# Performance work log

Measured on AMD Instinct MI355X. Metric: run time of the kernel, lower is better.

The kernel has to match this reference:

```python
import jax, jax.numpy as jnp
import numpy as np

HEADS = 4  # opt['heads']; attention_dim=128 -> d_k=32


def setup_inputs() -> dict:
    key = jax.random.key(0)
    ks = jax.random.split(key, 8)
    N, E, IN_F, ATT = 50000, 1600000, 256, 128
    x = jax.random.normal(ks[0], (N, IN_F), dtype=jnp.float32)
    edge = jax.random.randint(ks[1], (2, E), 0, N, dtype=jnp.int64)
    Qw = jax.random.normal(ks[2], (ATT, IN_F), dtype=jnp.float32) * 0.02
    Qb = jax.random.normal(ks[3], (ATT,), dtype=jnp.float32) * 0.02
    Kw = jax.random.normal(ks[4], (ATT, IN_F), dtype=jnp.float32) * 0.02
    Kb = jax.random.normal(ks[5], (ATT,), dtype=jnp.float32) * 0.02
    Vw = jax.random.normal(ks[6], (ATT, IN_F), dtype=jnp.float32) * 0.02
    Vb = jax.random.normal(ks[7], (ATT,), dtype=jnp.float32) * 0.02
    return {"x": x, "edge": edge, "Qw": Qw, "Qb": Qb, "Kw": Kw, "Kb": Kb, "Vw": Vw, "Vb": Vb}


def reference(x, edge, Qw, Qb, Kw, Kb, Vw, Vb):
    N = x.shape[0]
    att = Qw.shape[0]
    d_k = att // HEADS
    inv_sqrt_dk = np.float32(1.0 / np.sqrt(d_k))
    # projections, split into heads: [N, h, d_k]
    q = (x @ Qw.T + Qb).reshape(N, HEADS, d_k)
    k = (x @ Kw.T + Kb).reshape(N, HEADS, d_k)
    v = (x @ Vw.T + Vb).reshape(N, HEADS, d_k)
    src, dst = edge[0], edge[1]
    # per-edge dot-product scores over d_k: [E, h]
    scores = jnp.einsum('ehd,ehd->eh', q[src], k[dst]) * inv_sqrt_dk
    # segment softmax grouped by source node (edge[0])
    m = jax.ops.segment_max(scores, src, num_segments=N)  # [N, h]
    ex = jnp.exp(scores - m[src])
    denom = jax.ops.segment_sum(ex, src, num_segments=N)  # [N, h]
    attn = ex / denom[src]  # [E, h]
    # spmm per head: out[src] += attn * v[dst]; fused over heads
    out = jax.ops.segment_sum(attn[:, :, None] * v[dst], src, num_segments=N)  # [N, h, d_k]
    # torch cat over heads == head-major flatten
    return out.reshape(N, att)
```

## Files before the change

kernel.cpp:

```cpp
#include <hip/hip_runtime.h>

#define HEADS 4
#define ATT   128
#define INF   256
#define DK    32
#define KVROW 384
#define BSTRIDE 10240

typedef __attribute__((ext_vector_type(8))) short bf16x8;
typedef __attribute__((ext_vector_type(4))) float f32x4;
typedef __attribute__((ext_vector_type(2))) float f32x2;

__device__ __forceinline__ unsigned short f2bf(float f) {
    unsigned u = __float_as_uint(f);
    unsigned r = u + 0x7fffu + ((u >> 16) & 1u);
    return (unsigned short)(r >> 16);
}

__device__ __forceinline__ unsigned char f2fp8(float f) {
    return (unsigned char)(__builtin_amdgcn_cvt_pk_fp8_f32(f, f, 0, false) & 0xff);
}

__device__ __forceinline__ void gload_lds16(const void* g, void* s) {
    __builtin_amdgcn_global_load_lds(
        (const __attribute__((address_space(1))) void*)g,
        (__attribute__((address_space(3))) void*)s,
        16, 0, 0);
}

__global__ __launch_bounds__(256) void cast3_kernel(const float* __restrict__ a,
                                                    const float* __restrict__ b,
                                                    const float* __restrict__ c,
                                                    unsigned short* __restrict__ out, int n8) {
    const float* in = (blockIdx.y == 0) ? a : (blockIdx.y == 1) ? b : c;
    unsigned short* o = out + (size_t)blockIdx.y * n8 * 8;
    int stride = gridDim.x * 256;
    for (int i = blockIdx.x * 256 + threadIdx.x; i < n8; i += stride) {
        float4 p = ((const float4*)in)[(size_t)i * 2];
        float4 q = ((const float4*)in)[(size_t)i * 2 + 1];
        uint4 w;
        w.x = (unsigned)f2bf(p.x) | ((unsigned)f2bf(p.y) << 16);
        w.y = (unsigned)f2bf(p.z) | ((unsigned)f2bf(p.w) << 16);
        w.z = (unsigned)f2bf(q.x) | ((unsigned)f2bf(q.y) << 16);
        w.w = (unsigned)f2bf(q.z) | ((unsigned)f2bf(q.w) << 16);
        ((uint4*)o)[i] = w;
    }
}

__global__ __launch_bounds__(256) void proj_mfma(
    const float* __restrict__ x,
    const unsigned short* __restrict__ wb,
    const float* __restrict__ Bq, const float* __restrict__ Bk, const float* __restrict__ Bv,
    unsigned short* __restrict__ qout, unsigned char* __restrict__ kv, int N)
{
    __shared__ unsigned short As[128 * 32];
    __shared__ unsigned short Bs[128 * 32];

    const int t  = threadIdx.x;
    const int l  = t & 63;
    const int w  = t >> 6;
    const int wr = w >> 1, wc = w & 1;
    const int n0 = blockIdx.x * 128;
    const int mat = blockIdx.y;
    const unsigned short* W = wb + (size_t)mat * 128 * 256;

    f32x4 zero = {0.f, 0.f, 0.f, 0.f};
    f32x4 acc[4][4];
#pragma unroll
    for (int m = 0; m < 4; ++m)
#pragma unroll
        for (int n = 0; n < 4; ++n) acc[m][n] = zero;

    for (int k0 = 0; k0 < INF; k0 += 32) {
#pragma unroll
        for (int j = 0; j < 2; ++j) {
            int c = j * 256 + t;
            int row = c >> 2, part = c & 3;
            int gr = n0 + row; if (gr > N - 1) gr = N - 1;
            const float4* xp = (const float4*)&x[(size_t)gr * INF + k0 + part * 8];
            float4 a = xp[0], b = xp[1];
            uint4 o;
            o.x = (unsigned)f2bf(a.x) | ((unsigned)f2bf(a.y) << 16);
            o.y = (unsigned)f2bf(a.z) | ((unsigned)f2bf(a.w) << 16);
            o.z = (unsigned)f2bf(b.x) | ((unsigned)f2bf(b.y) << 16);
            o.w = (unsigned)f2bf(b.z) | ((unsigned)f2bf(b.w) << 16);
            *(uint4*)&As[(size_t)c * 8] = o;
        }
#pragma unroll
        for (int j = 0; j < 2; ++j) {
            int c = j * 256 + t;
            int row = c >> 2, part = c & 3;
            gload_lds16(W + (size_t)row * INF + k0 + part * 8,
                        &Bs[(size_t)(j * 256 + (w << 6)) * 8]);
        }
        __syncthreads();

        bf16x8 af[4], bfr[4];
#pragma unroll
        for (int m = 0; m < 4; ++m) {
            int row = wr * 64 + m * 16 + (l & 15);
            af[m] = *(const bf16x8*)&As[row * 32 + (l >> 4) * 8];
        }
#pragma unroll
        for (int n = 0; n < 4; ++n) {
            int row = wc * 64 + n * 16 + (l & 15);
            bfr[n] = *(const bf16x8*)&Bs[row * 32 + (l >> 4) * 8];
        }
#pragma unroll
        for (int m = 0; m < 4; ++m)
#pragma unroll
            for (int n = 0; n < 4; ++n)
                acc[m][n] = __builtin_amdgcn_mfma_f32_16x16x32_bf16(af[m], bfr[n], acc[m][n], 0, 0, 0);
        __syncthreads();
    }

    const float* bias = (mat == 0) ? Bq : ((mat == 1) ? Bk : Bv);

#pragma unroll
    for (int m = 0; m < 4; ++m) {
#pragma unroll
        for (int r = 0; r < 4; ++r) {
            int node = n0 + wr * 64 + m * 16 + (l >> 4) * 4 + r;
            if (node < N) {
                unsigned char* kvrow = kv + (size_t)node * KVROW;
#pragma unroll
                for (int n = 0; n < 4; ++n) {
                    int col = wc * 64 + n * 16 + (l & 15);
                    float val = acc[m][n][r] + bias[col];
                    if (mat == 0) {
                        qout[(size_t)node * ATT + col] = f2bf(val);
                    } else if (mat == 1) {
                        kvrow[col] = f2fp8(val * 16.0f);
                    } else {
                        *(unsigned short*)(kvrow + 128 + col * 2) = f2bf(val);
                    }
                }
            }
        }
    }
}

#define PCHUNK 4096
__global__ __launch_bounds__(256) void partA_kernel(const int* __restrict__ e32, int E,
                                                    int* __restrict__ gbcnt,
                                                    unsigned* __restrict__ eperm) {
    __shared__ int hist[256];
    __shared__ int lcur[256];
    __shared__ int s_is64;
    const int t = threadIdx.x;
    const int base = blockIdx.x * PCHUNK;

    if (t == 0) s_is64 = 1;
    hist[t] = 0;
    __syncthreads();
    if (e32[2 * t + 1] != 0) s_is64 = 0;
    __syncthreads();
    const int is64 = s_is64;

    int s[16], d[16];
    if (is64) {
#pragma unroll
        for (int j = 0; j < 8; ++j) {
            int e2 = base + j * 512 + 2 * t;
            s[2 * j] = -1; s[2 * j + 1] = -1; d[2 * j] = 0; d[2 * j + 1] = 0;
            if (e2 + 1 < E) {
                uint4 us = *(const uint4*)&e32[(size_t)2 * e2];
                uint4 ud = *(const uint4*)&e32[(size_t)2 * ((size_t)E + e2)];
                s[2 * j] = (int)us.x; d[2 * j] = (int)ud.x;
                s[2 * j + 1] = (int)us.z; d[2 * j + 1] = (int)ud.z;
            } else if (e2 < E) {
                s[2 * j] = e32[(size_t)2 * e2];
                d[2 * j] = e32[(size_t)2 * ((size_t)E + e2)];
            }
        }
    } else {
#pragma unroll
        for (int j = 0; j < 16; ++j) {
            int e = base + j * 256 + t;
            s[j] = -1; d[j] = 0;
            if (e < E) { s[j] = e32[e]; d[j] = e32[(size_t)E + e]; }
        }
    }
#pragma unroll
    for (int j = 0; j < 16; ++j)
        if (s[j] >= 0) atomicAdd(&hist[s[j] >> 8], 1);
    __syncthreads();
    int h = hist[t];
    int boff = 0;
    if (h > 0) boff = atomicAdd(&gbcnt[t], h);
    lcur[t] = t * BSTRIDE + boff;
    __syncthreads();
#pragma unroll
    for (int j = 0; j < 16; ++j) {
        if (s[j] >= 0) {
            int pos = atomicAdd(&lcur[s[j] >> 8], 1);
            eperm[pos] = ((unsigned)(s[j] & 255) << 16) | (unsigned)d[j];
        }
    }
}

__global__ __launch_bounds__(256) void partB_kernel(const unsigned* __restrict__ eperm,
                                                    const int* __restrict__ gbcnt,
                                                    uint2* __restrict__ off2,
                                                    int* __restrict__ sdst, int N) {
    __shared__ int hist[256];
    __shared__ int ws[4];
    __shared__ int lcur[256];
    const int b = blockIdx.x;
    const int t = threadIdx.x;
    const int lane = t & 63, w = t >> 6;
    const int base = b * BSTRIDE;
    const int cntb = gbcnt[b];

    hist[t] = 0;
    __syncthreads();
    for (int i = t; i < cntb; i += 256)
        atomicAdd(&hist[eperm[base + i] >> 16], 1);
    __syncthreads();

    int x = hist[t];
    int s = x;
#pragma unroll
    for (int d = 1; d < 64; d <<= 1) { int u = __shfl_up(s, d, 64); if (lane >= d) s += u; }
    if (lane == 63) ws[w] = s;
    __syncthreads();
    int carry = 0;
    for (int i = 0; i < w; ++i) carry += ws[i];
    int exc = carry + s - x;

    int node = (b << 8) + t;
    if (node < N) off2[node] = make_uint2((unsigned)(base + exc), (unsigned)(base + exc + x));
    lcur[t] = base + exc;
    __syncthreads();

    for (int i = t; i < cntb; i += 256) {
        unsigned p = eperm[base + i];
        int pos = atomicAdd(&lcur[p >> 16], 1);
        sdst[pos] = (int)(p & 0xffffu);
    }
}

__device__ __forceinline__ void pair_acc(unsigned kb, uint2 vv, bool live,
                                         float q0, float q1, float q2, float q3,
                                         float& o0, float& o1, float& o2, float& o3,
                                         float& den) {
    f32x2 k01 = __builtin_amdgcn_cvt_pk_f32_fp8((int)kb, false);
    f32x2 k23 = __builtin_amdgcn_cvt_pk_f32_fp8((int)kb, true);
    float part = fmaf(q0, k01[0], fmaf(q1, k01[1], fmaf(q2, k23[0], q3 * k23[1])));
    part += __shfl_xor(part, 1, 64);
    part += __shfl_xor(part, 2, 64);
    part += __shfl_xor(part, 4, 64);
    float p = live ? exp2f(part) : 0.f;
    den += p;
    float v0 = __uint_as_float(vv.x << 16);
    float v1 = __uint_as_float(vv.x & 0xffff0000u);
    float v2 = __uint_as_float(vv.y << 16);
    float v3 = __uint_as_float(vv.y & 0xffff0000u);
    o0 = fmaf(p, v0, o0);
    o1 = fmaf(p, v1, o1);
    o2 = fmaf(p, v2, o2);
    o3 = fmaf(p, v3, o3);
}

__global__ __launch_bounds__(256) void attn_kernel(
    const unsigned short* __restrict__ qb, const unsigned char* __restrict__ kv,
    const uint2* __restrict__ off2, const int* __restrict__ sdst,
    float* __restrict__ out, int N)
{
    const int wid = blockIdx.x * 4 + (threadIdx.x >> 6);
    const int l = threadIdx.x & 63;
    if (wid >= N) return;
    const uint2 oo = off2[wid];
    const int e0 = (int)oo.x, e1 = (int)oo.y;
    const int half = l >> 5, sub = l & 31;

    const float sc2 = 0.17677669529663687f * 1.4426950408889634f / 16.0f;
    uint2 qw = *(const uint2*)&qb[(size_t)wid * ATT + sub * 4];
    float q0 = __uint_as_float(qw.x << 16) * sc2;
    float q1 = __uint_as_float(qw.x & 0xffff0000u) * sc2;
    float q2 = __uint_as_float(qw.y << 16) * sc2;
    float q3 = __uint_as_float(qw.y & 0xffff0000u) * sc2;
    float o0 = 0.f, o1 = 0.f, o2 = 0.f, o3 = 0.f, den = 0.f;

    for (int base = e0; base < e1; base += 64) {
        int cnt = e1 - base; if (cnt > 64) cnt = 64;
        int dl = sdst[base + (l < cnt ? l : cnt - 1)];
        int j = 0;
        for (; j + 8 <= cnt; j += 8) {
            int d0 = __shfl(dl, j + half, 64);
            int d1 = __shfl(dl, j + 2 + half, 64);
            int d2 = __shfl(dl, j + 4 + half, 64);
            int d3 = __shfl(dl, j + 6 + half, 64);
            const unsigned char* r0 = kv + (size_t)d0 * KVROW;
            const unsigned char* r1 = kv + (size_t)d1 * KVROW;
            const unsigned char* r2 = kv + (size_t)d2 * KVROW;
            const unsigned char* r3 = kv + (size_t)d3 * KVROW;
            unsigned kb0 = *(const unsigned*)(r0 + sub * 4);
            uint2    vv0 = *(const uint2*)(r0 + 128 + sub * 8);
            unsigned kb1 = *(const unsigned*)(r1 + sub * 4);
            uint2    vv1 = *(const uint2*)(r1 + 128 + sub * 8);
            unsigned kb2 = *(const unsigned*)(r2 + sub * 4);
            uint2    vv2 = *(const uint2*)(r2 + 128 + sub * 8);
            unsigned kb3 = *(const unsigned*)(r3 + sub * 4);
            uint2    vv3 = *(const uint2*)(r3 + 128 + sub * 8);
            pair_acc(kb0, vv0, true, q0, q1, q2, q3, o0, o1, o2, o3, den);
            pair_acc(kb1, vv1, true, q0, q1, q2, q3, o0, o1, o2, o3, den);
            pair_acc(kb2, vv2, true, q0, q1, q2, q3, o0, o1, o2, o3, den);
            pair_acc(kb3, vv3, true, q0, q1, q2, q3, o0, o1, o2, o3, den);
        }
        for (; j + 4 <= cnt; j += 4) {
            int d0 = __shfl(dl, j + half, 64);
            int d1 = __shfl(dl, j + 2 + half, 64);
            const unsigned char* r0 = kv + (size_t)d0 * KVROW;
            const unsigned char* r1 = kv + (size_t)d1 * KVROW;
            unsigned kb0 = *(const unsigned*)(r0 + sub * 4);
            uint2    vv0 = *(const uint2*)(r0 + 128 + sub * 8);
            unsigned kb1 = *(const unsigned*)(r1 + sub * 4);
            uint2    vv1 = *(const uint2*)(r1 + 128 + sub * 8);
            pair_acc(kb0, vv0, true, q0, q1, q2, q3, o0, o1, o2, o3, den);
            pair_acc(kb1, vv1, true, q0, q1, q2, q3, o0, o1, o2, o3, den);
        }
        for (; j < cnt; j += 2) {
            int jj = j + half;
            int da = __shfl(dl, jj, 64);
            const unsigned char* r0 = kv + (size_t)da * KVROW;
            unsigned kb0 = *(const unsigned*)(r0 + sub * 4);
            uint2    vv0 = *(const uint2*)(r0 + 128 + sub * 8);
            pair_acc(kb0, vv0, jj < cnt, q0, q1, q2, q3, o0, o1, o2, o3, den);
        }
    }
    den += __shfl_xor(den, 32, 64);
    o0 += __shfl_xor(o0, 32, 64);
    o1 += __shfl_xor(o1, 32, 64);
    o2 += __shfl_xor(o2, 32, 64);
    o3 += __shfl_xor(o3, 32, 64);
    float r = (den > 0.f) ? 1.0f / den : 0.f;
    if (half == 0)
        *(float4*)&out[(size_t)wid * ATT + sub * 4] =
            make_float4(o0 * r, o1 * r, o2 * r, o3 * r);
}

extern "C" void kernel_launch(void* const* d_in, const int* in_sizes, int n_in,
                              void* d_out, int out_size, void* d_ws, size_t ws_size,
                              hipStream_t stream)
{
    const float* x   = (const float*)d_in[0];
    const int*   e32 = (const int*)d_in[1];
    const float* Wq  = (const float*)d_in[2];
    const float* Bq  = (const float*)d_in[3];
    const float* Wk  = (const float*)d_in[4];
    const float* Bk  = (const float*)d_in[5];
    const float* Wv  = (const float*)d_in[6];
    const float* Bv  = (const float*)d_in[7];
    float* out = (float*)d_out;

    const int N = in_sizes[0] / INF;
    const int E = in_sizes[1] / 2;

    char* ws = (char*)d_ws;
    size_t o = 0;
    auto take = [&](size_t bytes) -> char* {
        char* p = ws + o;
        o = (o + bytes + 255) & ~(size_t)255;
        return p;
    };
    unsigned short* wb = (unsigned short*)take((size_t)3 * ATT * INF * 2);
    unsigned short* qb = (unsigned short*)take((size_t)N * ATT * 2);
    unsigned char*  kv = (unsigned char*)take((size_t)N * KVROW);
    uint2* off2  = (uint2*)take((size_t)N * 8);
    int*   gbcnt = (int*)take(1024);
    unsigned* eperm = (unsigned*)take((size_t)256 * BSTRIDE * 4);
    int*   sdst  = (int*)take((size_t)256 * BSTRIDE * 4);
    (void)ws_size; (void)n_in; (void)out_size;

    const int nb = (N + 255) / 256;

    (void)hipMemsetAsync(gbcnt, 0, 1024, stream);
    cast3_kernel<<<dim3(16, 3), 256, 0, stream>>>(Wq, Wk, Wv, wb, (ATT * INF) / 8);

    proj_mfma<<<dim3((N + 127) / 128, 3), 256, 0, stream>>>(x, wb, Bq, Bk, Bv, qb, kv, N);

    partA_kernel<<<(E + PCHUNK - 1) / PCHUNK, 256, 0, stream>>>(e32, E, gbcnt, eperm);
    partB_kernel<<<nb, 256, 0, stream>>>(eperm, gbcnt, off2, sdst, N);

    attn_kernel<<<(N + 3) / 4, 256, 0, stream>>>(qb, kv, off2, sdst, out, N);
}
```

Measured before the change: 177.2 us.

## Fuse Q/K/V projections into one block and fold counter memset into cast

The projection kernel now computes all three Q, K and V matrices in one 384-thread block per 128-node tile, with each wave pair handling one matrix. The x tile is loaded and converted to bf16 once instead of three times, which removes redundant global reads of x. The bucket-counter memset is moved into the weight-cast kernel, dropping a separate API call. In exchange each wave holds twice as many accumulators (8x4 tiles), which raises register pressure and may lower occupancy, and LDS use for the B tile triples.

```diff
diff --git a/kernel.cpp b/kernel.cpp
--- a/kernel.cpp
+++ b/kernel.cpp
@@ -31,7 +31,9 @@
 __global__ __launch_bounds__(256) void cast3_kernel(const float* __restrict__ a,
                                                     const float* __restrict__ b,
                                                     const float* __restrict__ c,
-                                                    unsigned short* __restrict__ out, int n8) {
+                                                    unsigned short* __restrict__ out,
+                                                    int* __restrict__ gbcnt, int n8) {
+    if (blockIdx.x == 0 && blockIdx.y == 0) gbcnt[threadIdx.x] = 0;
     const float* in = (blockIdx.y == 0) ? a : (blockIdx.y == 1) ? b : c;
     unsigned short* o = out + (size_t)blockIdx.y * n8 * 8;
     int stride = gridDim.x * 256;
@@ -47,85 +49,83 @@
     }
 }
 
-__global__ __launch_bounds__(256) void proj_mfma(
+__global__ __launch_bounds__(384) void fproj_kernel(
     const float* __restrict__ x,
     const unsigned short* __restrict__ wb,
     const float* __restrict__ Bq, const float* __restrict__ Bk, const float* __restrict__ Bv,
     unsigned short* __restrict__ qout, unsigned char* __restrict__ kv, int N)
 {
     __shared__ unsigned short As[128 * 32];
-    __shared__ unsigned short Bs[128 * 32];
-
-    const int t  = threadIdx.x;
-    const int l  = t & 63;
-    const int w  = t >> 6;
-    const int wr = w >> 1, wc = w & 1;
-    const int n0 = blockIdx.x * 128;
-    const int mat = blockIdx.y;
-    const unsigned short* W = wb + (size_t)mat * 128 * 256;
+    __shared__ unsigned short Bs[3 * 128 * 32];
+
+    const int t   = threadIdx.x;
+    const int l   = t & 63;
+    const int w   = t >> 6;
+    const int mat = w >> 1;
+    const int ch  = w & 1;
+    const int n0  = blockIdx.x * 128;
 
     f32x4 zero = {0.f, 0.f, 0.f, 0.f};
-    f32x4 acc[4][4];
-#pragma unroll
-    for (int m = 0; m < 4; ++m)
+    f32x4 acc[8][4];
+#pragma unroll
+    for (int m = 0; m < 8; ++m)
 #pragma unroll
         for (int n = 0; n < 4; ++n) acc[m][n] = zero;
 
     for (int k0 = 0; k0 < INF; k0 += 32) {
 #pragma unroll
         for (int j = 0; j < 2; ++j) {
-            int c = j * 256 + t;
-            int row = c >> 2, part = c & 3;
-            int gr = n0 + row; if (gr > N - 1) gr = N - 1;
-            const float4* xp = (const float4*)&x[(size_t)gr * INF + k0 + part * 8];
-            float4 a = xp[0], b = xp[1];
-            uint4 o;
-            o.x = (unsigned)f2bf(a.x) | ((unsigned)f2bf(a.y) << 16);
-            o.y = (unsigned)f2bf(a.z) | ((unsigned)f2bf(a.w) << 16);
-            o.z = (unsigned)f2bf(b.x) | ((unsigned)f2bf(b.y) << 16);
-            o.w = (unsigned)f2bf(b.z) | ((unsigned)f2bf(b.w) << 16);
-            *(uint4*)&As[(size_t)c * 8] = o;
-        }
-#pragma unroll
-        for (int j = 0; j < 2; ++j) {
-            int c = j * 256 + t;
-            int row = c >> 2, part = c & 3;
-            gload_lds16(W + (size_t)row * INF + k0 + part * 8,
-                        &Bs[(size_t)(j * 256 + (w << 6)) * 8]);
+            int task = j * 384 + t;
+            if (task < 512) {
+                int row = task >> 2, part = task & 3;
+                int gr = n0 + row; if (gr > N - 1) gr = N - 1;
+                const float4* xp = (const float4*)&x[(size_t)gr * INF + k0 + part * 8];
+                float4 a = xp[0], b = xp[1];
+                uint4 o;
+                o.x = (unsigned)f2bf(a.x) | ((unsigned)f2bf(a.y) << 16);
+                o.y = (unsigned)f2bf(a.z) | ((unsigned)f2bf(a.w) << 16);
+                o.z = (unsigned)f2bf(b.x) | ((unsigned)f2bf(b.y) << 16);
+                o.w = (unsigned)f2bf(b.z) | ((unsigned)f2bf(b.w) << 16);
+                *(uint4*)&As[(size_t)task * 8] = o;
+            }
+        }
+#pragma unroll
+        for (int r = 0; r < 4; ++r) {
+            int task = r * 384 + t;
+            int mr = task >> 2, part = task & 3;
+            gload_lds16(wb + (size_t)mr * INF + k0 + part * 8,
+                        &Bs[(size_t)(r * 384 + w * 64) * 8]);
         }
         __syncthreads();
 
-        bf16x8 af[4], bfr[4];
-#pragma unroll
-        for (int m = 0; m < 4; ++m) {
-            int row = wr * 64 + m * 16 + (l & 15);
-            af[m] = *(const bf16x8*)&As[row * 32 + (l >> 4) * 8];
-        }
+        bf16x8 bfr[4];
 #pragma unroll
         for (int n = 0; n < 4; ++n) {
-            int row = wc * 64 + n * 16 + (l & 15);
-            bfr[n] = *(const bf16x8*)&Bs[row * 32 + (l >> 4) * 8];
-        }
-#pragma unroll
-        for (int m = 0; m < 4; ++m)
+            int row = mat * 128 + ch * 64 + n * 16 + (l & 15);
+            bfr[n] = *(const bf16x8*)&Bs[(size_t)row * 32 + (l >> 4) * 8];
+        }
+#pragma unroll
+        for (int m = 0; m < 8; ++m) {
+            bf16x8 af = *(const bf16x8*)&As[(size_t)(m * 16 + (l & 15)) * 32 + (l >> 4) * 8];
 #pragma unroll
             for (int n = 0; n < 4; ++n)
-                acc[m][n] = __builtin_amdgcn_mfma_f32_16x16x32_bf16(af[m], bfr[n], acc[m][n], 0, 0, 0);
+                acc[m][n] = __builtin_amdgcn_mfma_f32_16x16x32_bf16(af, bfr[n], acc[m][n], 0, 0, 0);
+        }
         __syncthreads();
     }
 
     const float* bias = (mat == 0) ? Bq : ((mat == 1) ? Bk : Bv);
 
 #pragma unroll
-    for (int m = 0; m < 4; ++m) {
+    for (int m = 0; m < 8; ++m) {
 #pragma unroll
         for (int r = 0; r < 4; ++r) {
-            int node = n0 + wr * 64 + m * 16 + (l >> 4) * 4 + r;
+            int node = n0 + m * 16 + (l >> 4) * 4 + r;
             if (node < N) {
                 unsigned char* kvrow = kv + (size_t)node * KVROW;
 #pragma unroll
                 for (int n = 0; n < 4; ++n) {
-                    int col = wc * 64 + n * 16 + (l & 15);
+                    int col = ch * 64 + n * 16 + (l & 15);
                     float val = acc[m][n][r] + bias[col];
                     if (mat == 0) {
                         qout[(size_t)node * ATT + col] = f2bf(val);
@@ -375,10 +375,9 @@
 
     const int nb = (N + 255) / 256;
 
-    (void)hipMemsetAsync(gbcnt, 0, 1024, stream);
-    cast3_kernel<<<dim3(16, 3), 256, 0, stream>>>(Wq, Wk, Wv, wb, (ATT * INF) / 8);
-
-    proj_mfma<<<dim3((N + 127) / 128, 3), 256, 0, stream>>>(x, wb, Bq, Bk, Bv, qb, kv, N);
+    cast3_kernel<<<dim3(16, 3), 256, 0, stream>>>(Wq, Wk, Wv, wb, gbcnt, (ATT * INF) / 8);
+
+    fproj_kernel<<<(N + 127) / 128, 384, 0, stream>>>(x, wb, Bq, Bk, Bv, qb, kv, N);
 
     partA_kernel<<<(E + PCHUNK - 1) / PCHUNK, 256, 0, stream>>>(e32, E, gbcnt, eperm);
     partB_kernel<<<nb, 256, 0, stream>>>(eperm, gbcnt, off2, sdst, N);
```

New measurement: 196.5 us. 10.9% more time.
